# Performance work log

Measured on AMD Instinct MI355X. Metric: run time of the kernel, lower is better.

The kernel has to match this reference:

```python
import jax
jax.config.update("jax_enable_x64", True)  # hash needs int64 like torch .long()
import jax.numpy as jnp
import numpy as np

N = 4_194_304
TABLE = 4096
EMB = 16
HID = 64


def setup_inputs() -> dict:
    key = jax.random.key(0)
    ks = jax.random.split(key, 9)
    pos = jax.random.normal(ks[0], (N, 3), jnp.float32)
    normal = jax.random.normal(ks[1], (N, 3), jnp.float32)
    emb = jax.random.normal(ks[2], (TABLE, EMB), jnp.float32) * 0.02
    W1 = jax.random.normal(ks[3], (EMB + 3, HID), jnp.float32) * (1.0 / np.sqrt(EMB + 3))
    b1 = jnp.zeros((HID,), jnp.float32)
    W2 = jax.random.normal(ks[4], (HID, HID), jnp.float32) * (1.0 / np.sqrt(HID))
    b2 = jnp.zeros((HID,), jnp.float32)
    W3 = jax.random.normal(ks[5], (HID, 3), jnp.float32) * (1.0 / np.sqrt(HID))
    b3 = jnp.zeros((3,), jnp.float32)
    return {"pos": pos, "normal": normal, "emb": emb,
            "W1": W1, "b1": b1, "W2": W2, "b2": b2, "W3": W3, "b3": b3}


def _hash_index(pos):
    # torch (pos*10).long() truncates toward zero; astype(int64) matches.
    scaled = (pos * 10.0).astype(jnp.int64)  # [N,3]
    h = (scaled[:, 0] * 73856093) ^ (scaled[:, 1] * 19349663) ^ (scaled[:, 2] * 83492791)
    # jnp.mod and torch % both return result with sign of divisor (nonneg here)
    return jnp.mod(h, TABLE)


def reference(pos, normal, emb, W1, b1, W2, b2, W3, b3):
    idx = _hash_index(pos)            # [N] int64 in [0, 4096)
    feat = emb[idx]                   # [N,16] gather
    x = jnp.concatenate([feat, normal], axis=-1)  # [N,19]
    h = jax.nn.relu(x @ W1 + b1)      # [N,64]
    h = jax.nn.relu(h @ W2 + b2)      # [N,64]
    return jax.nn.sigmoid(h @ W3 + b3)  # [N,3]
```

## Files before the change

kernel.cpp:

```cpp
#include <hip/hip_runtime.h>
#include <hip/hip_bf16.h>
#include <math.h>


typedef __attribute__((ext_vector_type(4)))  float        float4v;
typedef __attribute__((ext_vector_type(4)))  unsigned int uint4v;

#define WSF_OFF   0
#define WSB_OFF   (14 * 64 * 16)
#define EMB_OFF   (WSB_OFF + 5 * 64 * 16)

static __device__ __forceinline__ unsigned pack2_rne(float a, float b) {
    __hip_bfloat16 ha = __float2bfloat16(a), hb = __float2bfloat16(b);
    unsigned short ua = *reinterpret_cast<unsigned short*>(&ha);
    unsigned short ub = *reinterpret_cast<unsigned short*>(&hb);
    return (unsigned)ua | ((unsigned)ub << 16);
}
static __device__ __forceinline__ uint4v mk_frag_u(const float* v) {
    uint4v u;
    u.x = pack2_rne(v[0], v[1]); u.y = pack2_rne(v[2], v[3]);
    u.z = pack2_rne(v[4], v[5]); u.w = pack2_rne(v[6], v[7]);
    return u;
}
static __device__ __forceinline__ unsigned cvtpk(float a, float b) {
    unsigned r;
    asm("v_cvt_pk_bf16_f32 %0, %1, %2" : "=v"(r) : "v"(a), "v"(b));
    return r;
}
static __device__ __forceinline__ unsigned pkrelu(unsigned x) {
    unsigned r;
    asm("v_pk_max_i16 %0, %1, 0" : "=v"(r) : "v"(x));
    return r;
}

__global__ void nc_prep(const float* __restrict__ W1, const float* __restrict__ b1,
                        const float* __restrict__ W2, const float* __restrict__ b2,
                        const float* __restrict__ W3, const float* __restrict__ b3,
                        const float* __restrict__ emb, char* __restrict__ ws)
{
    uint4v*   wsf   = (uint4v*)(ws + WSF_OFF);
    float4v*  wsb   = (float4v*)(ws + WSB_OFF);
    unsigned* embbf = (unsigned*)(ws + EMB_OFF);

    const int gtid = blockIdx.x * blockDim.x + threadIdx.x;
    if (gtid < 32768)
        embbf[gtid] = pack2_rne(emb[2 * gtid], emb[2 * gtid + 1]);

    if (blockIdx.x != 0 || threadIdx.x >= 64) return;
    const int lane = threadIdx.x;
    const int m    = lane & 15;
    const int quad = lane >> 4;
    const int qs = m >> 2, rs = m & 3;

    for (int nt = 0; nt < 4; ++nt) {
        const int n = 32 * (nt >> 1) + 8 * qs + 4 * (nt & 1) + rs;
        float v[8];
        for (int j = 0; j < 8; ++j) {
            const int k = quad * 8 + j;
            v[j] = (k < 19) ? W1[k * 64 + n] : (k == 19 ? b1[n] : 0.0f);
        }
        wsf[nt * 64 + lane] = mk_frag_u(v);
    }
    for (int kt = 0; kt < 2; ++kt)
        for (int nt = 0; nt < 4; ++nt) {
            const int n = 32 * (nt >> 1) + 8 * qs + 4 * (nt & 1) + rs;
            float v[8];
            for (int j = 0; j < 8; ++j)
                v[j] = W2[(kt * 32 + quad * 8 + j) * 64 + n];
            wsf[(4 + kt * 4 + nt) * 64 + lane] = mk_frag_u(v);
        }
    for (int kt = 0; kt < 2; ++kt) {
        float v[8];
        for (int j = 0; j < 8; ++j)
            v[j] = (m < 3) ? W3[(kt * 32 + quad * 8 + j) * 3 + m] : 0.0f;
        wsf[(12 + kt) * 64 + lane] = mk_frag_u(v);
    }
    for (int nt = 0; nt < 4; ++nt) {
        const int base = 32 * (nt >> 1) + 8 * quad + 4 * (nt & 1);
        float4v v; v.x = b2[base]; v.y = b2[base+1]; v.z = b2[base+2]; v.w = b2[base+3];
        wsb[nt * 64 + lane] = v;
    }
    float4v v3;
    v3.x = (quad == 0) ? b3[0] : 0.f;
    v3.y = (quad == 0) ? b3[1] : 0.f;
    v3.z = (quad == 0) ? b3[2] : 0.f;
    v3.w = 0.f;
    wsb[4 * 64 + lane] = v3;
}

__global__ __launch_bounds__(256, 4) void nc_mfma10(
    const float* __restrict__ pos, const float* __restrict__ nrm,
    const char* __restrict__ ws, float* __restrict__ out, int npts)
{
    const uint4v*  wsf   = (const uint4v*)(ws + WSF_OFF);
    const float4v* wsb   = (const float4v*)(ws + WSB_OFF);
    const char*    embbf = ws + EMB_OFF;

    const int lane = threadIdx.x & 63;
    const int m    = lane & 15;
    const int quad = lane >> 4;

    uint4v w1p[4], w2p[2][4], w3p[2];
    float4v b2p[4], b3p;
    float4v zerof = (float4v){0.f, 0.f, 0.f, 0.f};
    #pragma unroll
    for (int nt = 0; nt < 4; ++nt) w1p[nt] = wsf[nt * 64 + lane];
    #pragma unroll
    for (int kt = 0; kt < 2; ++kt)
        #pragma unroll
        for (int nt = 0; nt < 4; ++nt)
            w2p[kt][nt] = wsf[(4 + kt * 4 + nt) * 64 + lane];
    #pragma unroll
    for (int kt = 0; kt < 2; ++kt) w3p[kt] = wsf[(12 + kt) * 64 + lane];
    #pragma unroll
    for (int nt = 0; nt < 4; ++nt) b2p[nt] = wsb[nt * 64 + lane];
    b3p = wsb[4 * 64 + lane];

    asm volatile("" : "+a"(w1p[0]), "+a"(w1p[1]), "+a"(w1p[2]), "+a"(w1p[3]));
    asm volatile("" : "+a"(w2p[0][0]), "+a"(w2p[0][1]), "+a"(w2p[0][2]), "+a"(w2p[0][3]));
    asm volatile("" : "+a"(w2p[1][0]), "+a"(w2p[1][1]), "+a"(w2p[1][2]), "+a"(w2p[1][3]));
    asm volatile("" : "+a"(w3p[0]), "+a"(w3p[1]));
    asm volatile("" : "+v"(b2p[0]), "+v"(b2p[1]), "+v"(b2p[2]), "+v"(b2p[3]));
    asm volatile("" : "+v"(b3p), "+v"(zerof));

    const int groupsTotal = npts >> 6;
    const int waveId      = blockIdx.x * 4 + (threadIdx.x >> 6);
    const int numWaves    = gridDim.x * 4;

    const int  a0   = m << 2;
    const bool is2  = (quad == 2);
    const int  esel = (quad & 1) << 4;

    int g = waveId;
    float p0 = 0.f, p1 = 0.f, p2 = 0.f, n0 = 0.f, n1 = 0.f, n2 = 0.f;
    if (g < groupsTotal) {
        const int pt = g * 64 + lane;
        p0 = pos[3 * pt + 0]; p1 = pos[3 * pt + 1]; p2 = pos[3 * pt + 2];
        n0 = nrm[3 * pt + 0]; n1 = nrm[3 * pt + 1]; n2 = nrm[3 * pt + 2];
    }

    for (; g < groupsTotal; g += numWaves) {
        const int base3 = g * 192;

        const int sx = (int)(p0 * 10.0f);
        const int sy = (int)(p1 * 10.0f);
        const int sz = (int)(p2 * 10.0f);
        const unsigned h = ((unsigned)sx * 73856093u)
                         ^ ((unsigned)sy * 19349663u)
                         ^ ((unsigned)sz * 83492791u);
        const int idxb = (int)((h & 4095u) << 5);

        const unsigned np0 = cvtpk(n0, n1);
        const unsigned np1 = cvtpk(n2, 1.0f);

        {
            const int tn  = g + numWaves;
            const int ptn = ((tn < groupsTotal) ? tn : g) * 64 + lane;
            p0 = pos[3 * ptn + 0]; p1 = pos[3 * ptn + 1]; p2 = pos[3 * ptn + 2];
            n0 = nrm[3 * ptn + 0]; n1 = nrm[3 * ptn + 1]; n2 = nrm[3 * ptn + 2];
        }

        int      eoffc = __builtin_amdgcn_ds_bpermute(a0, idxb);
        unsigned p0c   = (unsigned)__builtin_amdgcn_ds_bpermute(a0, (int)np0);
        unsigned p1c   = (unsigned)__builtin_amdgcn_ds_bpermute(a0, (int)np1);
        uint4v   exc   = *(const uint4v*)(embbf + eoffc + esel);

        #pragma unroll 1
        for (int j = 0; j < 4; ++j) {
            const int bn = a0 + ((((j + 1) & 3)) << 6);
            const int      eoffn = __builtin_amdgcn_ds_bpermute(bn, idxb);
            const unsigned p0n   = (unsigned)__builtin_amdgcn_ds_bpermute(bn, (int)np0);
            const unsigned p1n   = (unsigned)__builtin_amdgcn_ds_bpermute(bn, (int)np1);
            const uint4v   exn   = *(const uint4v*)(embbf + eoffn + esel);

            uint4v xu;
            xu.x = is2 ? p0c : exc.x;
            xu.y = is2 ? p1c : exc.y;
            xu.z = exc.z;
            xu.w = exc.w;

            float4v h1_0, h1_1, h1_2, h1_3;
            asm("s_nop 1\n\t"
                "v_mfma_f32_16x16x32_bf16 %0, %4, %8, %9\n\t"
                "v_mfma_f32_16x16x32_bf16 %1, %5, %8, %9\n\t"
                "v_mfma_f32_16x16x32_bf16 %2, %6, %8, %9\n\t"
                "v_mfma_f32_16x16x32_bf16 %3, %7, %8, %9\n\t"
                "s_nop 7\n\ts_nop 7"
                : "=&v"(h1_0), "=&v"(h1_1), "=&v"(h1_2), "=&v"(h1_3)
                : "a"(w1p[0]), "a"(w1p[1]), "a"(w1p[2]), "a"(w1p[3]),
                  "v"(xu), "v"(zerof));

            uint4v B10, B11;
            B10.x = pkrelu(cvtpk(h1_0.x, h1_0.y));
            B10.y = pkrelu(cvtpk(h1_0.z, h1_0.w));
            B10.z = pkrelu(cvtpk(h1_1.x, h1_1.y));
            B10.w = pkrelu(cvtpk(h1_1.z, h1_1.w));
            B11.x = pkrelu(cvtpk(h1_2.x, h1_2.y));
            B11.y = pkrelu(cvtpk(h1_2.z, h1_2.w));
            B11.z = pkrelu(cvtpk(h1_3.x, h1_3.y));
            B11.w = pkrelu(cvtpk(h1_3.z, h1_3.w));

            float4v h2_0, h2_1, h2_2, h2_3;
            asm("s_nop 1\n\t"
                "v_mfma_f32_16x16x32_bf16 %0, %4, %12, %14\n\t"
                "v_mfma_f32_16x16x32_bf16 %1, %5, %12, %15\n\t"
                "v_mfma_f32_16x16x32_bf16 %2, %6, %12, %16\n\t"
                "v_mfma_f32_16x16x32_bf16 %3, %7, %12, %17\n\t"
                "v_mfma_f32_16x16x32_bf16 %0, %8, %13, %0\n\t"
                "v_mfma_f32_16x16x32_bf16 %1, %9, %13, %1\n\t"
                "v_mfma_f32_16x16x32_bf16 %2, %10, %13, %2\n\t"
                "v_mfma_f32_16x16x32_bf16 %3, %11, %13, %3\n\t"
                "s_nop 7\n\ts_nop 7"
                : "=&v"(h2_0), "=&v"(h2_1), "=&v"(h2_2), "=&v"(h2_3)
                : "a"(w2p[0][0]), "a"(w2p[0][1]), "a"(w2p[0][2]), "a"(w2p[0][3]),
                  "a"(w2p[1][0]), "a"(w2p[1][1]), "a"(w2p[1][2]), "a"(w2p[1][3]),
                  "v"(B10), "v"(B11),
                  "v"(b2p[0]), "v"(b2p[1]), "v"(b2p[2]), "v"(b2p[3]));

            uint4v B20, B21;
            B20.x = pkrelu(cvtpk(h2_0.x, h2_0.y));
            B20.y = pkrelu(cvtpk(h2_0.z, h2_0.w));
            B20.z = pkrelu(cvtpk(h2_1.x, h2_1.y));
            B20.w = pkrelu(cvtpk(h2_1.z, h2_1.w));
            B21.x = pkrelu(cvtpk(h2_2.x, h2_2.y));
            B21.y = pkrelu(cvtpk(h2_2.z, h2_2.w));
            B21.z = pkrelu(cvtpk(h2_3.x, h2_3.y));
            B21.w = pkrelu(cvtpk(h2_3.z, h2_3.w));

            float4v lg;
            asm("s_nop 1\n\t"
                "v_mfma_f32_16x16x32_bf16 %0, %1, %3, %5\n\t"
                "v_mfma_f32_16x16x32_bf16 %0, %2, %4, %0\n\t"
                "s_nop 7\n\ts_nop 7"
                : "=&v"(lg)
                : "a"(w3p[0]), "a"(w3p[1]), "v"(B20), "v"(B21), "v"(b3p));

            if (quad == 0) {
                const float a0f = lg.x * -1.44269504f;
                const float a1f = lg.y * -1.44269504f;
                const float a2f = lg.z * -1.44269504f;
                float s0, s1, s2;
                asm("v_exp_f32 %0, %3\n\t"
                    "v_exp_f32 %1, %4\n\t"
                    "v_exp_f32 %2, %5\n\t"
                    "v_add_f32 %0, 1.0, %0\n\t"
                    "v_add_f32 %1, 1.0, %1\n\t"
                    "v_add_f32 %2, 1.0, %2\n\t"
                    "v_rcp_f32 %0, %0\n\t"
                    "v_rcp_f32 %1, %1\n\t"
                    "v_rcp_f32 %2, %2\n\t"
                    "s_nop 0"
                    : "=&v"(s0), "=&v"(s1), "=&v"(s2)
                    : "v"(a0f), "v"(a1f), "v"(a2f));
                float* o = out + base3 + j * 48 + 3 * m;
                o[0] = s0; o[1] = s1; o[2] = s2;
            }

            exc = exn; p0c = p0n; p1c = p1n;
        }
    }
}

extern "C" void kernel_launch(void* const* d_in, const int* in_sizes, int n_in,
                              void* d_out, int out_size, void* d_ws, size_t ws_size,
                              hipStream_t stream) {
    const float* pos = (const float*)d_in[0];
    const float* nrm = (const float*)d_in[1];
    const float* emb = (const float*)d_in[2];
    const float* W1  = (const float*)d_in[3];
    const float* b1  = (const float*)d_in[4];
    const float* W2  = (const float*)d_in[5];
    const float* b2  = (const float*)d_in[6];
    const float* W3  = (const float*)d_in[7];
    const float* b3  = (const float*)d_in[8];
    float* out = (float*)d_out;

    const int npts = in_sizes[0] / 3;

    nc_prep<<<128, 256, 0, stream>>>(W1, b1, W2, b2, W3, b3, emb, (char*)d_ws);
    nc_mfma10<<<1024, 256, 0, stream>>>(pos, nrm, (const char*)d_ws, out, npts);
}
```

Measured before the change: 218.2 us.

## Software-pipeline sigmoid into next layer-2 MFMA and prefetch hash across groups

The sigmoid epilogue (exp/add/rcp) for the previous 16-point tile is deferred and interleaved between the layer-2 MFMA instructions of the next tile, so transcendental ALU work hides under matrix-core latency. The hash and normal packing for the next group is computed inside the last inner iteration, and the first embedding gather is hoisted ahead of the loop, so the gather is pipelined across group boundaries. The catch is extra live registers and a separate epilogue block for the final tile. Sigmoid now runs on all quads rather than only quad 0, which is redundant work.

Result: slower. 566.4 us (+159.6%).

```diff
diff --git a/kernel.cpp b/kernel.cpp
--- a/kernel.cpp
+++ b/kernel.cpp
@@ -88,7 +88,7 @@
     wsb[4 * 64 + lane] = v3;
 }
 
-__global__ __launch_bounds__(256, 4) void nc_mfma10(
+__global__ __launch_bounds__(256, 4) void nc_mfma12(
     const float* __restrict__ pos, const float* __restrict__ nrm,
     const char* __restrict__ ws, float* __restrict__ out, int npts)
 {
@@ -139,19 +139,22 @@
         n0 = nrm[3 * pt + 0]; n1 = nrm[3 * pt + 1]; n2 = nrm[3 * pt + 2];
     }
 
+    int sx = (int)(p0 * 10.0f), sy = (int)(p1 * 10.0f), sz = (int)(p2 * 10.0f);
+    unsigned hh = ((unsigned)sx * 73856093u) ^ ((unsigned)sy * 19349663u)
+                ^ ((unsigned)sz * 83492791u);
+    int      idxb = (int)((hh & 4095u) << 5);
+    unsigned np0  = cvtpk(n0, n1);
+    unsigned np1  = cvtpk(n2, 1.0f);
+
+    int      eoffc = __builtin_amdgcn_ds_bpermute(a0, idxb);
+    unsigned p0c   = (unsigned)__builtin_amdgcn_ds_bpermute(a0, (int)np0);
+    unsigned p1c   = (unsigned)__builtin_amdgcn_ds_bpermute(a0, (int)np1);
+    uint4v   exc   = *(const uint4v*)(embbf + eoffc + esel);
+
+    float4v lgp = zerof;
+
     for (; g < groupsTotal; g += numWaves) {
         const int base3 = g * 192;
-
-        const int sx = (int)(p0 * 10.0f);
-        const int sy = (int)(p1 * 10.0f);
-        const int sz = (int)(p2 * 10.0f);
-        const unsigned h = ((unsigned)sx * 73856093u)
-                         ^ ((unsigned)sy * 19349663u)
-                         ^ ((unsigned)sz * 83492791u);
-        const int idxb = (int)((h & 4095u) << 5);
-
-        const unsigned np0 = cvtpk(n0, n1);
-        const unsigned np1 = cvtpk(n2, 1.0f);
 
         {
             const int tn  = g + numWaves;
@@ -160,13 +163,17 @@
             n0 = nrm[3 * ptn + 0]; n1 = nrm[3 * ptn + 1]; n2 = nrm[3 * ptn + 2];
         }
 
-        int      eoffc = __builtin_amdgcn_ds_bpermute(a0, idxb);
-        unsigned p0c   = (unsigned)__builtin_amdgcn_ds_bpermute(a0, (int)np0);
-        unsigned p1c   = (unsigned)__builtin_amdgcn_ds_bpermute(a0, (int)np1);
-        uint4v   exc   = *(const uint4v*)(embbf + eoffc + esel);
-
         #pragma unroll 1
         for (int j = 0; j < 4; ++j) {
+            if (j == 3) {
+                sx = (int)(p0 * 10.0f); sy = (int)(p1 * 10.0f); sz = (int)(p2 * 10.0f);
+                hh = ((unsigned)sx * 73856093u) ^ ((unsigned)sy * 19349663u)
+                   ^ ((unsigned)sz * 83492791u);
+                idxb = (int)((hh & 4095u) << 5);
+                np0  = cvtpk(n0, n1);
+                np1  = cvtpk(n2, 1.0f);
+            }
+
             const int bn = a0 + ((((j + 1) & 3)) << 6);
             const int      eoffn = __builtin_amdgcn_ds_bpermute(bn, idxb);
             const unsigned p0n   = (unsigned)__builtin_amdgcn_ds_bpermute(bn, (int)np0);
@@ -200,22 +207,37 @@
             B11.z = pkrelu(cvtpk(h1_3.x, h1_3.y));
             B11.w = pkrelu(cvtpk(h1_3.z, h1_3.w));
 
+            const float a0f = lgp.x * -1.44269504f;
+            const float a1f = lgp.y * -1.44269504f;
+            const float a2f = lgp.z * -1.44269504f;
             float4v h2_0, h2_1, h2_2, h2_3;
+            float s0, s1, s2;
             asm("s_nop 1\n\t"
-                "v_mfma_f32_16x16x32_bf16 %0, %4, %12, %14\n\t"
-                "v_mfma_f32_16x16x32_bf16 %1, %5, %12, %15\n\t"
-                "v_mfma_f32_16x16x32_bf16 %2, %6, %12, %16\n\t"
-                "v_mfma_f32_16x16x32_bf16 %3, %7, %12, %17\n\t"
-                "v_mfma_f32_16x16x32_bf16 %0, %8, %13, %0\n\t"
-                "v_mfma_f32_16x16x32_bf16 %1, %9, %13, %1\n\t"
-                "v_mfma_f32_16x16x32_bf16 %2, %10, %13, %2\n\t"
-                "v_mfma_f32_16x16x32_bf16 %3, %11, %13, %3\n\t"
+                "v_mfma_f32_16x16x32_bf16 %0, %7, %15, %17\n\t"
+                "v_exp_f32 %4, %21\n\t"
+                "v_mfma_f32_16x16x32_bf16 %1, %8, %15, %18\n\t"
+                "v_exp_f32 %5, %22\n\t"
+                "v_mfma_f32_16x16x32_bf16 %2, %9, %15, %19\n\t"
+                "v_exp_f32 %6, %23\n\t"
+                "v_mfma_f32_16x16x32_bf16 %3, %10, %15, %20\n\t"
+                "v_add_f32 %4, 1.0, %4\n\t"
+                "v_mfma_f32_16x16x32_bf16 %0, %11, %16, %0\n\t"
+                "v_add_f32 %5, 1.0, %5\n\t"
+                "v_mfma_f32_16x16x32_bf16 %1, %12, %16, %1\n\t"
+                "v_add_f32 %6, 1.0, %6\n\t"
+                "v_mfma_f32_16x16x32_bf16 %2, %13, %16, %2\n\t"
+                "v_rcp_f32 %4, %4\n\t"
+                "v_mfma_f32_16x16x32_bf16 %3, %14, %16, %3\n\t"
+                "v_rcp_f32 %5, %5\n\t"
+                "v_rcp_f32 %6, %6\n\t"
                 "s_nop 7\n\ts_nop 7"
-                : "=&v"(h2_0), "=&v"(h2_1), "=&v"(h2_2), "=&v"(h2_3)
+                : "=&v"(h2_0), "=&v"(h2_1), "=&v"(h2_2), "=&v"(h2_3),
+                  "=&v"(s0), "=&v"(s1), "=&v"(s2)
                 : "a"(w2p[0][0]), "a"(w2p[0][1]), "a"(w2p[0][2]), "a"(w2p[0][3]),
                   "a"(w2p[1][0]), "a"(w2p[1][1]), "a"(w2p[1][2]), "a"(w2p[1][3]),
                   "v"(B10), "v"(B11),
-                  "v"(b2p[0]), "v"(b2p[1]), "v"(b2p[2]), "v"(b2p[3]));
+                  "v"(b2p[0]), "v"(b2p[1]), "v"(b2p[2]), "v"(b2p[3]),
+                  "v"(a0f), "v"(a1f), "v"(a2f));
 
             uint4v B20, B21;
             B20.x = pkrelu(cvtpk(h2_0.x, h2_0.y));
@@ -235,28 +257,36 @@
                 : "=&v"(lg)
                 : "a"(w3p[0]), "a"(w3p[1]), "v"(B20), "v"(B21), "v"(b3p));
 
-            if (quad == 0) {
-                const float a0f = lg.x * -1.44269504f;
-                const float a1f = lg.y * -1.44269504f;
-                const float a2f = lg.z * -1.44269504f;
-                float s0, s1, s2;
-                asm("v_exp_f32 %0, %3\n\t"
-                    "v_exp_f32 %1, %4\n\t"
-                    "v_exp_f32 %2, %5\n\t"
-                    "v_add_f32 %0, 1.0, %0\n\t"
-                    "v_add_f32 %1, 1.0, %1\n\t"
-                    "v_add_f32 %2, 1.0, %2\n\t"
-                    "v_rcp_f32 %0, %0\n\t"
-                    "v_rcp_f32 %1, %1\n\t"
-                    "v_rcp_f32 %2, %2\n\t"
-                    "s_nop 0"
-                    : "=&v"(s0), "=&v"(s1), "=&v"(s2)
-                    : "v"(a0f), "v"(a1f), "v"(a2f));
-                float* o = out + base3 + j * 48 + 3 * m;
+            if (j != 0 && quad == 0) {
+                float* o = out + base3 + (j - 1) * 48 + 3 * m;
                 o[0] = s0; o[1] = s1; o[2] = s2;
             }
 
+            lgp = lg;
             exc = exn; p0c = p0n; p1c = p1n;
+        }
+
+        {
+            const float a0f = lgp.x * -1.44269504f;
+            const float a1f = lgp.y * -1.44269504f;
+            const float a2f = lgp.z * -1.44269504f;
+            float s0, s1, s2;
+            asm("v_exp_f32 %0, %3\n\t"
+                "v_exp_f32 %1, %4\n\t"
+                "v_exp_f32 %2, %5\n\t"
+                "v_add_f32 %0, 1.0, %0\n\t"
+                "v_add_f32 %1, 1.0, %1\n\t"
+                "v_add_f32 %2, 1.0, %2\n\t"
+                "v_rcp_f32 %0, %0\n\t"
+                "v_rcp_f32 %1, %1\n\t"
+                "v_rcp_f32 %2, %2\n\t"
+                "s_nop 0"
+                : "=&v"(s0), "=&v"(s1), "=&v"(s2)
+                : "v"(a0f), "v"(a1f), "v"(a2f));
+            if (quad == 0) {
+                float* o = out + base3 + 144 + 3 * m;
+                o[0] = s0; o[1] = s1; o[2] = s2;
+            }
         }
     }
 }
@@ -278,5 +308,5 @@
     const int npts = in_sizes[0] / 3;
 
     nc_prep<<<128, 256, 0, stream>>>(W1, b1, W2, b2, W3, b3, emb, (char*)d_ws);
-    nc_mfma10<<<1024, 256, 0, stream>>>(pos, nrm, (const char*)d_ws, out, npts);
-}
+    nc_mfma12<<<1024, 256, 0, stream>>>(pos, nrm, (const char*)d_ws, out, npts);
+}
```
